# Kernel tuning notes

Hardware: AMD Instinct MI355X
Metric: run time of the kernel (lower is better)

The kernel has to match this reference:

```python
import jax, jax.numpy as jnp
import numpy as np

B, L, DM, H, DH = 2, 2048, 1024, 4, 128
TOT = H * DH  # 512


def _dwconv(x, w, b, L):
    # x: (B,L,C), w: (C,1,4) depthwise, padding=3 then causal trim to L (matches Conv1d(padding=3)[...,:L])
    y = jax.lax.conv_general_dilated(x.transpose(0, 2, 1), w, (1,), [(3, 3)],
                                     dimension_numbers=('NCH', 'OIH', 'NCH'),
                                     feature_group_count=w.shape[0])
    y = y[..., :L] + b[None, :, None]
    return y.transpose(0, 2, 1)


def _l2norm(x):
    return x / jnp.maximum(jnp.linalg.norm(x, axis=-1, keepdims=True), 1e-12)


def setup_inputs() -> dict:
    key = jax.random.key(0)
    ks = jax.random.split(key, 16)
    s = 0.02
    return {
        'x': jax.random.normal(ks[0], (B, L, DM), jnp.float32),
        'state': jnp.zeros((B, H, DH, DH), jnp.float32),
        'Wq': jax.random.normal(ks[1], (TOT, DM), jnp.float32) * s,
        'Wk': jax.random.normal(ks[2], (TOT, DM), jnp.float32) * s,
        'Wv': jax.random.normal(ks[3], (2 * TOT, DM), jnp.float32) * s,
        'Wa': jax.random.normal(ks[4], (H, DM), jnp.float32) * s,
        'Wb': jax.random.normal(ks[5], (H, DM), jnp.float32) * s,
        'Wg': jax.random.normal(ks[6], (TOT, DM), jnp.float32) * s,
        'Wo': jax.random.normal(ks[7], (DM, TOT), jnp.float32) * s,
        'qcw': jax.random.normal(ks[8], (TOT, 1, 4), jnp.float32) * 0.1,
        'qcb': jnp.zeros((TOT,), jnp.float32),
        'kcw': jax.random.normal(ks[9], (TOT, 1, 4), jnp.float32) * 0.1,
        'kcb': jnp.zeros((TOT,), jnp.float32),
        'vcw': jax.random.normal(ks[10], (2 * TOT, 1, 4), jnp.float32) * 0.1,
        'vcb': jnp.zeros((2 * TOT,), jnp.float32),
        'ln_w': jnp.ones((TOT,), jnp.float32),
        'ln_b': jnp.zeros((TOT,), jnp.float32),
    }


def reference(x, state, Wq, Wk, Wv, Wa, Wb, Wg, Wo, qcw, qcb, kcw, kcb, vcw, vcb, ln_w, ln_b):
    Bn, Ln, _ = x.shape
    q = _dwconv(x @ Wq.T, qcw, qcb, Ln)
    k = _dwconv(x @ Wk.T, kcw, kcb, Ln)
    v = _dwconv(x @ Wv.T, vcw, vcb, Ln)
    # silu then L2-normalize over the FULL total_dim (before head split), as in the source
    q = _l2norm(jax.nn.silu(q))
    k = _l2norm(jax.nn.silu(k))
    v = jax.nn.silu(v)
    alpha = jax.nn.sigmoid(x @ Wa.T)  # (B,L,H)
    beta = jax.nn.sigmoid(x @ Wb.T)   # (B,L,H)
    q = q.reshape(Bn, Ln, H, DH)
    k = k.reshape(Bn, Ln, H, DH)
    v_main, v_gate = jnp.split(v, 2, axis=-1)
    v_main = v_main.reshape(Bn, Ln, H, DH)
    v_gate = v_gate.reshape(Bn, Ln, H, DH)

    def step(S, inp):
        q_t, k_t, v_t, a_t, b_t = inp  # (B,H,D),(B,H,D),(B,H,D),(B,H),(B,H)
        a = a_t[..., None, None]
        b = b_t[..., None, None]
        Sk = jnp.einsum('bhij,bhj->bhi', S, k_t)  # S @ k
        # S @ (alpha*(I - beta k k^T)) + beta v k^T, via rank-1 update
        S = a * (S - b * (Sk[..., :, None] * k_t[..., None, :])) \
            + b * (v_t[..., :, None] * k_t[..., None, :])
        o = jnp.einsum('bhij,bhj->bhi', S, q_t)
        return S, o

    xs = (q.transpose(1, 0, 2, 3), k.transpose(1, 0, 2, 3), v_main.transpose(1, 0, 2, 3),
          alpha.transpose(1, 0, 2), beta.transpose(1, 0, 2))
    final_state, outs = jax.lax.scan(step, state, xs)
    out = outs.transpose(1, 0, 2, 3)  # (B,L,H,D)

    out = (out * v_gate).reshape(Bn, Ln, TOT)
    out = out * jax.nn.silu(x @ Wg.T)
    mu = out.mean(-1, keepdims=True)
    var = jnp.mean((out - mu) ** 2, axis=-1, keepdims=True)
    out = (out - mu) * jax.lax.rsqrt(var + 1e-5) * ln_w + ln_b
    out = out @ Wo.T
    return out, final_state
```

## Files before the change

### kernel.cpp

```cpp
#include <hip/hip_runtime.h>
#include <hip/hip_bf16.h>

#define BQ    2
#define LQ    2048
#define DMQ   1024
#define HQ    4
#define DHQ   128
#define TOTQ  512
#define BLQ   4096
#define NPROJ 2688
#define KPROJ 1024
#define CT    64
#define NCH   32

typedef short bf16x8 __attribute__((ext_vector_type(8)));
typedef short s16x4  __attribute__((ext_vector_type(4)));
typedef float f32x4  __attribute__((ext_vector_type(4)));

#define MFMA16(a, b, c) __builtin_amdgcn_mfma_f32_16x16x32_bf16(a, b, c, 0, 0, 0)

__device__ __forceinline__ float siluf(float x) { return x / (1.f + __expf(-x)); }
__device__ __forceinline__ float sigf(float x)  { return 1.f / (1.f + __expf(-x)); }
__device__ __forceinline__ short bf16s(float x) {
  return __builtin_bit_cast(short, __float2bfloat16(x));
}
__device__ __forceinline__ bf16x8 pack8(f32x4 a, f32x4 b) {
  bf16x8 r;
  r[0] = bf16s(a.x); r[1] = bf16s(a.y); r[2] = bf16s(a.z); r[3] = bf16s(a.w);
  r[4] = bf16s(b.x); r[5] = bf16s(b.y); r[6] = bf16s(b.z); r[7] = bf16s(b.w);
  return r;
}

__device__ __forceinline__ void gload_lds16(const void* g, void* l) {
  __builtin_amdgcn_global_load_lds(
      (__attribute__((address_space(1))) void*)(unsigned long long)g,
      (__attribute__((address_space(3))) void*)(unsigned int)(unsigned long long)l,
      16, 0, 0);
}

__global__ __launch_bounds__(256)
void cast_f32_bf16_kernel(const float* __restrict__ src, __hip_bfloat16* __restrict__ dst, int n4)
{
  int i = blockIdx.x * 256 + threadIdx.x;
  if (i < n4) {
    float4 v = ((const float4*)src)[i];
    __hip_bfloat16 o[4] = { __float2bfloat16(v.x), __float2bfloat16(v.y),
                            __float2bfloat16(v.z), __float2bfloat16(v.w) };
    *(ushort4*)((unsigned short*)dst + (size_t)i * 4) = *(ushort4*)o;
  }
}

__global__ __launch_bounds__(256)
void cast_wcat_kernel(const float* __restrict__ Wq, const float* __restrict__ Wk,
                      const float* __restrict__ Wv, const float* __restrict__ Wg,
                      const float* __restrict__ Wa, const float* __restrict__ Wb,
                      __hip_bfloat16* __restrict__ Wcat)
{
  int i4 = blockIdx.x * 256 + threadIdx.x;
  int row = i4 >> 8;
  int col = (i4 & 255) * 4;
  int idx = row * 1024 + col;
  float4 v;
  if      (row < 512)  v = *(const float4*)(Wq + idx);
  else if (row < 1024) v = *(const float4*)(Wk + idx - 512 * 1024);
  else if (row < 2048) v = *(const float4*)(Wv + idx - 1024 * 1024);
  else if (row < 2560) v = *(const float4*)(Wg + idx - 2048 * 1024);
  else if (row < 2564) v = *(const float4*)(Wa + (row - 2560) * 1024 + col);
  else if (row < 2568) v = *(const float4*)(Wb + (row - 2564) * 1024 + col);
  else                 v = make_float4(0.f, 0.f, 0.f, 0.f);
  __hip_bfloat16 o[4] = { __float2bfloat16(v.x), __float2bfloat16(v.y),
                          __float2bfloat16(v.z), __float2bfloat16(v.w) };
  *(ushort4*)((unsigned short*)Wcat + idx) = *(ushort4*)o;
}

__global__ __launch_bounds__(256)
void gemm_bt_kernel(const __hip_bfloat16* __restrict__ A,
                    const __hip_bfloat16* __restrict__ Bw,
                    float* __restrict__ C, int M, int N, int K)
{
  __shared__ __hip_bfloat16 As[2 * 128 * 32];
  __shared__ __hip_bfloat16 Bs[2 * 128 * 32];
  const int tid  = threadIdx.x;
  const int lane = tid & 63;
  const int w    = tid >> 6;
  const int wm   = w >> 1, wn = w & 1;
  const int tm   = blockIdx.x, tn = blockIdx.y;
  const int lr   = lane & 15, lk = lane >> 4;

  f32x4 acc[4][4] = {};

  const int e0   = tid * 8;
  const int srow = e0 >> 5;
  const int scol = e0 & 31;
  const __hip_bfloat16* Ap = A  + (size_t)(tm * 128 + srow) * K + scol;
  const __hip_bfloat16* Bp = Bw + (size_t)(tn * 128 + srow) * K + scol;
  char* AsB  = (char*)As;
  char* BsB  = (char*)Bs;
  const size_t half = (size_t)64 * K;
  const int nk = K >> 5;

  {
    char* AsD = AsB + w * 1024;
    char* BsD = BsB + w * 1024;
    gload_lds16(Ap,        AsD);
    gload_lds16(Ap + half, AsD + 4096);
    gload_lds16(Bp,        BsD);
    gload_lds16(Bp + half, BsD + 4096);
  }
  __syncthreads();

  for (int it = 0; it < nk; ++it) {
    const int sel = it & 1;
    if (it + 1 < nk) {
      const int kk = (it + 1) * 32;
      char* AsD = AsB + ((sel ^ 1) * 8192) + w * 1024;
      char* BsD = BsB + ((sel ^ 1) * 8192) + w * 1024;
      gload_lds16(Ap + kk,        AsD);
      gload_lds16(Ap + half + kk, AsD + 4096);
      gload_lds16(Bp + kk,        BsD);
      gload_lds16(Bp + half + kk, BsD + 4096);
    }
    const char* AsR = AsB + sel * 8192;
    const char* BsR = BsB + sel * 8192;
    bf16x8 af[4], bfv[4];
#pragma unroll
    for (int m = 0; m < 4; ++m)
      af[m]  = *(const bf16x8*)(AsR + ((wm * 64 + m * 16 + lr) * 32 + lk * 8) * 2);
#pragma unroll
    for (int n = 0; n < 4; ++n)
      bfv[n] = *(const bf16x8*)(BsR + ((wn * 64 + n * 16 + lr) * 32 + lk * 8) * 2);
#pragma unroll
    for (int m = 0; m < 4; ++m)
#pragma unroll
      for (int n = 0; n < 4; ++n)
        acc[m][n] = MFMA16(af[m], bfv[n], acc[m][n]);
    __syncthreads();
  }

  const int crow0 = tm * 128 + wm * 64 + (lane >> 4) * 4;
  const int ccol0 = tn * 128 + wn * 64 + lr;
#pragma unroll
  for (int m = 0; m < 4; ++m)
#pragma unroll
    for (int n = 0; n < 4; ++n)
#pragma unroll
      for (int j = 0; j < 4; ++j)
        C[(size_t)(crow0 + m * 16 + j) * N + ccol0 + n * 16] = acc[m][n][j];
}

__global__ __launch_bounds__(256)
void conv_act_kernel(const float* __restrict__ C,
                     const float* __restrict__ qcw, const float* __restrict__ qcb,
                     const float* __restrict__ kcw, const float* __restrict__ kcb,
                     const float* __restrict__ vcw, const float* __restrict__ vcb,
                     float* __restrict__ qh, float* __restrict__ kh,
                     float* __restrict__ vm, float* __restrict__ vg,
                     float* __restrict__ al, float* __restrict__ be)
{
  const int blk = blockIdx.x;
  const int bl0 = blk * 8;
  const int t0  = bl0 & (LQ - 1);
  const int tid = threadIdx.x;
  __shared__ float red[4][16];

  float2 qv[8], kv[8];
  float sq[8], sk[8];
#pragma unroll
  for (int t = 0; t < 8; ++t) { sq[t] = 0.f; sk[t] = 0.f; }

  {
    const int c0 = tid * 2;
    const float4 wqA = *(const float4*)(qcw + 4 * c0);
    const float4 wqB = *(const float4*)(qcw + 4 * c0 + 4);
    const float4 wkA = *(const float4*)(kcw + 4 * c0);
    const float4 wkB = *(const float4*)(kcw + 4 * c0 + 4);
    const float2 bq = *(const float2*)(qcb + c0);
    const float2 bk = *(const float2*)(kcb + c0);
    float2 wrq[11], wrk[11];
#pragma unroll
    for (int r = 0; r < 11; ++r) {
      const int tt = t0 - 3 + r;
      if (tt >= 0) {
        const float* Cr = C + (size_t)(bl0 - 3 + r) * NPROJ;
        wrq[r] = *(const float2*)(Cr + c0);
        wrk[r] = *(const float2*)(Cr + 512 + c0);
      } else {
        wrq[r] = make_float2(0.f, 0.f);
        wrk[r] = make_float2(0.f, 0.f);
      }
    }
#pragma unroll
    for (int t = 0; t < 8; ++t) {
      float aq0 = bq.x, aq1 = bq.y, ak0 = bk.x, ak1 = bk.y;
#pragma unroll
      for (int j = 0; j < 4; ++j) {
        aq0 = fmaf(((const float*)&wqA)[j], wrq[t + j].x, aq0);
        aq1 = fmaf(((const float*)&wqB)[j], wrq[t + j].y, aq1);
        ak0 = fmaf(((const float*)&wkA)[j], wrk[t + j].x, ak0);
        ak1 = fmaf(((const float*)&wkB)[j], wrk[t + j].y, ak1);
      }
      const float q0 = siluf(aq0), q1 = siluf(aq1);
      const float k0 = siluf(ak0), k1 = siluf(ak1);
      qv[t] = make_float2(q0, q1);
      kv[t] = make_float2(k0, k1);
      sq[t] = fmaf(q1, q1, fmaf(q0, q0, sq[t]));
      sk[t] = fmaf(k1, k1, fmaf(k0, k0, sk[t]));
    }
  }
#pragma unroll
  for (int m = 1; m < 64; m <<= 1) {
#pragma unroll
    for (int t = 0; t < 8; ++t) {
      sq[t] += __shfl_xor(sq[t], m);
      sk[t] += __shfl_xor(sk[t], m);
    }
  }
  {
    const int w = tid >> 6, lane = tid & 63;
    if (lane == 0) {
#pragma unroll
      for (int t = 0; t < 8; ++t) { red[w][t] = sq[t]; red[w][8 + t] = sk[t]; }
    }
  }
  __syncthreads();
  float rnq[8], rnk[8];
#pragma unroll
  for (int t = 0; t < 8; ++t) {
    const float SQ = red[0][t] + red[1][t] + red[2][t] + red[3][t];
    const float SK = red[0][8 + t] + red[1][8 + t] + red[2][8 + t] + red[3][8 + t];
    rnq[t] = 1.f / fmaxf(sqrtf(SQ), 1e-12f);
    rnk[t] = 1.f / fmaxf(sqrtf(SK), 1e-12f);
  }
  {
    const int c0 = tid * 2;
#pragma unroll
    for (int t = 0; t < 8; ++t) {
      *(float2*)(qh + (size_t)(bl0 + t) * 512 + c0) =
          make_float2(qv[t].x * rnq[t], qv[t].y * rnq[t]);
      *(float2*)(kh + (size_t)(bl0 + t) * 512 + c0) =
          make_float2(kv[t].x * rnk[t], kv[t].y * rnk[t]);
    }
  }
  {
    const int cv = tid * 4;
    const float4 wv0 = *(const float4*)(vcw + 4 * cv);
    const float4 wv1 = *(const float4*)(vcw + 4 * cv + 4);
    const float4 wv2 = *(const float4*)(vcw + 4 * cv + 8);
    const float4 wv3 = *(const float4*)(vcw + 4 * cv + 12);
    const float4 bv4 = *(const float4*)(vcb + cv);
    float4 wr[11];
#pragma unroll
    for (int r = 0; r < 11; ++r) {
      const int tt = t0 - 3 + r;
      wr[r] = (tt >= 0) ? *(const float4*)(C + (size_t)(bl0 - 3 + r) * NPROJ + 1024 + cv)
                        : make_float4(0.f, 0.f, 0.f, 0.f);
    }
#pragma unroll
    for (int t = 0; t < 8; ++t) {
      float a0 = bv4.x, a1 = bv4.y, a2 = bv4.z, a3 = bv4.w;
#pragma unroll
      for (int j = 0; j < 4; ++j) {
        a0 = fmaf(((const float*)&wv0)[j], ((const float*)&wr[t + j])[0], a0);
        a1 = fmaf(((const float*)&wv1)[j], ((const float*)&wr[t + j])[1], a1);
        a2 = fmaf(((const float*)&wv2)[j], ((const float*)&wr[t + j])[2], a2);
        a3 = fmaf(((const float*)&wv3)[j], ((const float*)&wr[t + j])[3], a3);
      }
      const float4 o = make_float4(siluf(a0), siluf(a1), siluf(a2), siluf(a3));
      if (cv < 512) *(float4*)(vm + (size_t)(bl0 + t) * 512 + cv)         = o;
      else          *(float4*)(vg + (size_t)(bl0 + t) * 512 + (cv - 512)) = o;
    }
  }
  if (tid < 64) {
    const int t = tid >> 3;
    const int k = tid & 7;
    const float* Cr = C + (size_t)(bl0 + t) * NPROJ;
    if (k < 4) al[(size_t)(bl0 + t) * 4 + k]       = sigf(Cr[2560 + k]);
    else       be[(size_t)(bl0 + t) * 4 + (k - 4)] = sigf(Cr[2564 + (k - 4)]);
  }
}

__global__ __launch_bounds__(256)
void scan_phaseA_kernel(const float* __restrict__ qh, const float* __restrict__ kh,
                        const float* __restrict__ vm, const float* __restrict__ al,
                        const float* __restrict__ be,
                        short* __restrict__ WTB, short* __restrict__ ZB,
                        short* __restrict__ PHB, short* __restrict__ KTB,
                        float* __restrict__ GV, float* __restrict__ GC,
                        short* __restrict__ WTFB, short* __restrict__ ZFB)
{
  __shared__ char sm[83968];
  float* Xl = (float*)(sm);
  __hip_bfloat16* KBl = (__hip_bfloat16*)(sm);
  __hip_bfloat16* QBl = (__hip_bfloat16*)(sm + 17408);
  float* Ll  = (float*)(sm + 65536);
  float* dv  = (float*)(sm + 82944);
  float* bv  = (float*)(sm + 83200);
  float* gbv = (float*)(sm + 83456);
  float* fvs = (float*)(sm + 83712);

  const int cb = blockIdx.x;
  const int bh = cb & 7, c = cb >> 3;
  const int b = bh >> 2, h = bh & 3;
  const int tid = threadIdx.x;
  const int lane = tid & 63;
  const int w = tid >> 6;
  const int lr = lane & 15, lk = lane >> 4;
  const size_t rowbase = (size_t)(b * LQ + c * CT) * 512 + h * 128;

#pragma unroll
  for (int rep = 0; rep < 4; ++rep) {
    const int fid = tid + rep * 256;
    const int r = fid >> 4;
    const int cg = (fid & 15) * 8;
    const float* kp = kh + rowbase + (size_t)r * 512 + cg;
    const float* qp = qh + rowbase + (size_t)r * 512 + cg;
    f32x4 k0 = *(const f32x4*)kp, k1 = *(const f32x4*)(kp + 4);
    f32x4 q0 = *(const f32x4*)qp, q1 = *(const f32x4*)(qp + 4);
    *(bf16x8*)(KBl + r * 136 + cg) = pack8(k0, k1);
    *(bf16x8*)(QBl + r * 136 + cg) = pack8(q0, q1);
  }
  if (w == 0) {
    float la = __logf(al[(size_t)(b * LQ + c * CT + lane) * 4 + h]);
    const float bb = be[(size_t)(b * LQ + c * CT + lane) * 4 + h];
#pragma unroll
    for (int off = 1; off < 64; off <<= 1) {
      const float tv = __shfl_up(la, off, 64);
      if (lane >= off) la += tv;
    }
    const float d63 = __shfl(la, 63, 64);
    dv[lane] = la; bv[lane] = bb; gbv[lane] = bb * __expf(la);
    fvs[lane] = __expf(d63 - la);
    GV[cb * 64 + lane] = __expf(la);
    if (lane == 0) GC[cb] = __expf(d63);
  }
  __syncthreads();

  f32x4 aG[4] = {}, aP[4] = {};
#pragma unroll
  for (int ks = 0; ks < 4; ++ks) {
    bf16x8 bk[4];
#pragma unroll
    for (int nt = 0; nt < 4; ++nt)
      bk[nt] = *(const bf16x8*)(KBl + (nt * 16 + lr) * 136 + ks * 32 + lk * 8);
    const bf16x8 ak = *(const bf16x8*)(KBl + (w * 16 + lr) * 136 + ks * 32 + lk * 8);
    const bf16x8 aq = *(const bf16x8*)(QBl + (w * 16 + lr) * 136 + ks * 32 + lk * 8);
#pragma unroll
    for (int nt = 0; nt < 4; ++nt) {
      aG[nt] = MFMA16(ak, bk[nt], aG[nt]);
      aP[nt] = MFMA16(aq, bk[nt], aP[nt]);
    }
  }
#pragma unroll
  for (int nt = 0; nt < 4; ++nt)
#pragma unroll
    for (int jj = 0; jj < 4; ++jj) {
      const int t = w * 16 + lk * 4 + jj;
      const int s = nt * 16 + lr;
      const float eg = __expf(dv[t] - dv[s]);
      Ll[t * 68 + s] = (t > s) ? bv[t] * eg * aG[nt][jj] : 0.f;
      PHB[(size_t)cb * 4096 + t * 64 + s] = (s <= t) ? bf16s(eg * aP[nt][jj]) : (short)0;
    }
  __syncthreads();

  const int j = tid;
  const float* src = (j < 128) ? kh : vm;
  const float* xp = src + rowbase + (j & 127);
  float* XlC = Xl + j;
  short* dstN = (j < 128) ? (WTB + (size_t)cb * 8192 + j)
                          : (ZB  + (size_t)cb * 8192 + (j - 128));
  short* dstT = (j < 128) ? (WTFB + (size_t)cb * 8192 + (size_t)j * 64)
                          : (ZFB  + (size_t)cb * 8192 + (size_t)(j - 128) * 64);

  for (int r = 0; r < 4; ++r) {
    float u[16];
#pragma unroll
    for (int i = 0; i < 16; ++i) {
      const int t = r * 16 + i;
      u[i] = xp[(size_t)t * 512] * ((j < 128) ? gbv[t] : bv[t]);
    }
    for (int sc = 0; sc < r; ++sc) {
      float xs[16];
#pragma unroll
      for (int k = 0; k < 16; ++k) xs[k] = XlC[(sc * 16 + k) * 256];
#pragma unroll
      for (int i = 0; i < 16; ++i) {
        const float* lrow = Ll + (r * 16 + i) * 68 + sc * 16;
        const f32x4 l0 = *(const f32x4*)(lrow);
        const f32x4 l1 = *(const f32x4*)(lrow + 4);
        const f32x4 l2 = *(const f32x4*)(lrow + 8);
        const f32x4 l3 = *(const f32x4*)(lrow + 12);
        f32x4 acc = {};
        acc.x = fmaf(l0.x, xs[0],  acc.x); acc.y = fmaf(l0.y, xs[1],  acc.y);
        acc.z = fmaf(l0.z, xs[2],  acc.z); acc.w = fmaf(l0.w, xs[3],  acc.w);
        acc.x = fmaf(l1.x, xs[4],  acc.x); acc.y = fmaf(l1.y, xs[5],  acc.y);
        acc.z = fmaf(l1.z, xs[6],  acc.z); acc.w = fmaf(l1.w, xs[7],  acc.w);
        acc.x = fmaf(l2.x, xs[8],  acc.x); acc.y = fmaf(l2.y, xs[9],  acc.y);
        acc.z = fmaf(l2.z, xs[10], acc.z); acc.w = fmaf(l2.w, xs[11], acc.w);
        acc.x = fmaf(l3.x, xs[12], acc.x); acc.y = fmaf(l3.y, xs[13], acc.y);
        acc.z = fmaf(l3.z, xs[14], acc.z); acc.w = fmaf(l3.w, xs[15], acc.w);
        u[i] -= (acc.x + acc.y) + (acc.z + acc.w);
      }
    }
#pragma unroll
    for (int i = 1; i < 16; ++i) {
      const float* lrow = Ll + (r * 16 + i) * 68 + r * 16;
      f32x4 acc = {};
#pragma unroll
      for (int k4 = 0; k4 < 4; ++k4) {
        if (k4 * 4 < i) {
          const f32x4 lv = *(const f32x4*)(lrow + k4 * 4);
          acc.x = fmaf(lv.x, u[k4 * 4 + 0], acc.x);
          acc.y = fmaf(lv.y, u[k4 * 4 + 1], acc.y);
          acc.z = fmaf(lv.z, u[k4 * 4 + 2], acc.z);
          acc.w = fmaf(lv.w, u[k4 * 4 + 3], acc.w);
        }
      }
      u[i] -= (acc.x + acc.y) + (acc.z + acc.w);
    }
    if (r < 3) {
#pragma unroll
      for (int i = 0; i < 16; ++i) XlC[(r * 16 + i) * 256] = u[i];
    }
#pragma unroll
    for (int i = 0; i < 16; ++i)
      dstN[(r * 16 + i) * 128] = bf16s(u[i]);
#pragma unroll
    for (int s4 = 0; s4 < 4; ++s4) {
      s16x4 p;
#pragma unroll
      for (int e = 0; e < 4; ++e)
        p[e] = bf16s(fvs[r * 16 + s4 * 4 + e] * u[s4 * 4 + e]);
      *(s16x4*)(dstT + r * 16 + s4 * 4) = p;
    }
  }

  if (tid < 128) {
    const float* kp2 = kh + rowbase + tid;
#pragma unroll
    for (int s4 = 0; s4 < 16; ++s4) {
      s16x4 pk;
#pragma unroll
      for (int e = 0; e < 4; ++e)
        pk[e] = bf16s(kp2[(size_t)(s4 * 4 + e) * 512]);
      *(s16x4*)(KTB + (size_t)cb * 8192 + tid * 64 + s4 * 4) = pk;
    }
  }
}

__global__ __launch_bounds__(256)
void scan_transition_kernel(const short* __restrict__ WTFB, const short* __restrict__ ZFB,
                            const short* __restrict__ KTB, const float* __restrict__ GC,
                            short* __restrict__ TRB, float* __restrict__ BF)
{
  const int cb = blockIdx.x;
  const int tid = threadIdx.x, lane = tid & 63, w = tid >> 6;
  const int lr = lane & 15, lk = lane >> 4;
  const float gc = GC[cb];

  {
    f32x4 acc[2][8] = {};
#pragma unroll
    for (int ks = 0; ks < 2; ++ks) {
      bf16x8 a0 = *(const bf16x8*)(KTB + (size_t)cb * 8192 + (w * 32 + lr) * 64 + ks * 32 + lk * 8);
      bf16x8 a1 = *(const bf16x8*)(KTB + (size_t)cb * 8192 + (w * 32 + 16 + lr) * 64 + ks * 32 + lk * 8);
#pragma unroll
      for (int nt = 0; nt < 8; ++nt) {
        const bf16x8 bm = *(const bf16x8*)(WTFB + (size_t)cb * 8192 + (nt * 16 + lr) * 64 + ks * 32 + lk * 8);
        acc[0][nt] = MFMA16(a0, bm, acc[0][nt]);
        acc[1][nt] = MFMA16(a1, bm, acc[1][nt]);
      }
    }
#pragma unroll
    for (int mt = 0; mt < 2; ++mt)
#pragma unroll
      for (int nt = 0; nt < 8; ++nt)
#pragma unroll
        for (int jj = 0; jj < 4; ++jj) {
          const int jr = w * 32 + mt * 16 + lk * 4 + jj;
          const int m  = nt * 16 + lr;
          const float v = ((jr == m) ? gc : 0.f) - acc[mt][nt][jj];
          TRB[(size_t)cb * 16384 + jr * 128 + m] = bf16s(v);
        }
  }
  {
    f32x4 acc[2][8] = {};
#pragma unroll
    for (int ks = 0; ks < 2; ++ks) {
      bf16x8 a0 = *(const bf16x8*)(ZFB + (size_t)cb * 8192 + (w * 32 + lr) * 64 + ks * 32 + lk * 8);
      bf16x8 a1 = *(const bf16x8*)(ZFB + (size_t)cb * 8192 + (w * 32 + 16 + lr) * 64 + ks * 32 + lk * 8);
#pragma unroll
      for (int nt = 0; nt < 8; ++nt) {
        const bf16x8 bj = *(const bf16x8*)(KTB + (size_t)cb * 8192 + (nt * 16 + lr) * 64 + ks * 32 + lk * 8);
        acc[0][nt] = MFMA16(a0, bj, acc[0][nt]);
        acc[1][nt] = MFMA16(a1, bj, acc[1][nt]);
      }
    }
#pragma unroll
    for (int mt = 0; mt < 2; ++mt)
#pragma unroll
      for (int nt = 0; nt < 8; ++nt)
#pragma unroll
        for (int jj = 0; jj < 4; ++jj) {
          const int ir = w * 32 + mt * 16 + lk * 4 + jj;
          const int jc = nt * 16 + lr;
          BF[(size_t)cb * 16384 + ir * 128 + jc] = acc[mt][nt][jj];
        }
  }
}

#define L2_PREFETCH(BT, BA, CC) do {                                               \
  const int cbn_ = (CC) * 8 + bh;                                                  \
  _Pragma("unroll") for (int nt = 0; nt < 2; ++nt) {                               \
    _Pragma("unroll") for (int ks = 0; ks < 4; ++ks)                               \
      BT[nt][ks] = *(const bf16x8*)(TRB + (size_t)cbn_ * 16384 +                   \
                                    (w * 32 + nt * 16 + lr) * 128 + ks * 32 + lk * 8); \
    _Pragma("unroll") for (int jj = 0; jj < 4; ++jj)                               \
      BA[nt][jj] = BF[(size_t)cbn_ * 16384 + (r0 + lk * 4 + jj) * 128 +            \
                      w * 32 + nt * 16 + lr];                                      \
  }                                                                                \
} while (0)

#define L2_STEP(BT, BA, CC, PBT, PBA) do {                                         \
  const int cb_ = (CC) * 8 + bh;                                                   \
  { const int idx = tid * 8, r = idx >> 7, jc = idx & 127;                         \
    f32x4 s0 = *(const f32x4*)&Scur[r * 132 + jc];                                 \
    f32x4 s1 = *(const f32x4*)&Scur[r * 132 + jc + 4];                             \
    *(bf16x8*)(SALL + (size_t)cb_ * 16384 + (r0 + r) * 128 + jc) = pack8(s0, s1); }\
  bf16x8 af[4];                                                                    \
  _Pragma("unroll") for (int ks = 0; ks < 4; ++ks)                                 \
    af[ks] = pack8(*(const f32x4*)&Scur[lr * 132 + ks * 32 + lk * 8],              \
                   *(const f32x4*)&Scur[lr * 132 + ks * 32 + lk * 8 + 4]);         \
  if ((CC) < 31) L2_PREFETCH(PBT, PBA, (CC) + 1);                                  \
  f32x4 acc0 = {}, acc1 = {};                                                      \
  _Pragma("unroll") for (int ks = 0; ks < 4; ++ks) {                               \
    acc0 = MFMA16(af[ks], BT[0][ks], acc0);                                        \
    acc1 = MFMA16(af[ks], BT[1][ks], acc1);                                        \
  }                                                                                \
  _Pragma("unroll") for (int jj = 0; jj < 4; ++jj) {                               \
    Snxt[(lk * 4 + jj) * 132 + w * 32 + lr]      = acc0[jj] + BA[0][jj];           \
    Snxt[(lk * 4 + jj) * 132 + w * 32 + 16 + lr] = acc1[jj] + BA[1][jj];           \
  }                                                                                \
  __syncthreads();                                                                 \
  { float* t_ = Scur; Scur = Snxt; Snxt = t_; }                                    \
} while (0)

__global__ __launch_bounds__(256)
void scan_state_kernel(const short* __restrict__ TRB, const float* __restrict__ BF,
                       const float* __restrict__ st0, short* __restrict__ SALL,
                       float* __restrict__ stout)
{
  __shared__ float Sl[2 * 16 * 132];
  const int bid = blockIdx.x;
  const int bh = bid & 7, slab = bid >> 3;
  const int r0 = slab * 16;
  const int tid = threadIdx.x, lane = tid & 63, w = tid >> 6;
  const int lr = lane & 15, lk = lane >> 4;

  float* Scur = Sl;
  float* Snxt = Sl + 16 * 132;

  {
    const int idx = tid * 8, r = idx >> 7, jc = idx & 127;
    const float* sp = st0 + ((size_t)bh * 128 + r0 + r) * 128 + jc;
    *(f32x4*)&Scur[r * 132 + jc]     = *(const f32x4*)sp;
    *(f32x4*)&Scur[r * 132 + jc + 4] = *(const f32x4*)(sp + 4);
  }
  bf16x8 btA[2][4], btB[2][4];
  float  baA[2][4], baB[2][4];
  L2_PREFETCH(btA, baA, 0);
  __syncthreads();

  for (int c2 = 0; c2 < 16; ++c2) {
    L2_STEP(btA, baA, 2 * c2,     btB, baB);
    L2_STEP(btB, baB, 2 * c2 + 1, btA, baA);
  }

  {
    const int idx = tid * 8, r = idx >> 7, jc = idx & 127;
    float* sp = stout + ((size_t)bh * 128 + r0 + r) * 128 + jc;
    *(f32x4*)sp       = *(const f32x4*)&Scur[r * 132 + jc];
    *(f32x4*)(sp + 4) = *(const f32x4*)&Scur[r * 132 + jc + 4];
  }
}

__global__ __launch_bounds__(512)
void scan_output_kernel(const float* __restrict__ qh,
                        const short* __restrict__ WTB, const __hip_bfloat16* __restrict__ ZB,
                        const short* __restrict__ PHB, const float* __restrict__ GV,
                        const short* __restrict__ SALL, float* __restrict__ obuf)
{
  __shared__ short Ut[128 * 72];
  const int cb = blockIdx.x;
  const int bh = cb & 7, c = cb >> 3;
  const int b = bh >> 2, h = bh & 3;
  const int tid = threadIdx.x, lane = tid & 63, w = tid >> 6;
  const int lr = lane & 15, lk = lane >> 4;
  const int r0 = (w & 3) * 16;

  f32x4 Y[8] = {};
#pragma unroll
  for (int ks = 0; ks < 4; ++ks) {
    bf16x8 af;
    if (w < 4) {
      const float* qp = qh + ((size_t)(b * LQ + c * CT) + r0 + lr) * 512 + h * 128 + ks * 32 + lk * 8;
      af = pack8(*(const f32x4*)qp, *(const f32x4*)(qp + 4));
    } else {
      af = *(const bf16x8*)(WTB + (size_t)cb * 8192 + (r0 + lr) * 128 + ks * 32 + lk * 8);
    }
#pragma unroll
    for (int nt = 0; nt < 8; ++nt) {
      const bf16x8 bs = *(const bf16x8*)(SALL + (size_t)cb * 16384 + (nt * 16 + lr) * 128 + ks * 32 + lk * 8);
      Y[nt] = MFMA16(af, bs, Y[nt]);
    }
  }
  if (w >= 4) {
#pragma unroll
    for (int nt = 0; nt < 8; ++nt) {
      const int i = nt * 16 + lr;
      s16x4 up;
#pragma unroll
      for (int jj = 0; jj < 4; ++jj) {
        const int s = r0 + lk * 4 + jj;
        const float z = __bfloat162float(ZB[(size_t)cb * 8192 + s * 128 + i]);
        up[jj] = bf16s(z - Y[nt][jj]);
      }
      *(s16x4*)&Ut[i * 72 + r0 + lk * 4] = up;
    }
  }
  __syncthreads();
  if (w < 4) {
    f32x4 P2[8] = {};
#pragma unroll
    for (int ks = 0; ks < 2; ++ks) {
      const bf16x8 ap = *(const bf16x8*)(PHB + (size_t)cb * 4096 + (r0 + lr) * 64 + ks * 32 + lk * 8);
#pragma unroll
      for (int nt = 0; nt < 8; ++nt) {
        const bf16x8 bu = *(const bf16x8*)&Ut[(nt * 16 + lr) * 72 + ks * 32 + lk * 8];
        P2[nt] = MFMA16(ap, bu, P2[nt]);
      }
    }
    float gvv[4];
#pragma unroll
    for (int jj = 0; jj < 4; ++jj) gvv[jj] = GV[cb * 64 + r0 + lk * 4 + jj];
#pragma unroll
    for (int nt = 0; nt < 8; ++nt) {
      const int i = nt * 16 + lr;
#pragma unroll
      for (int jj = 0; jj < 4; ++jj) {
        const int t = r0 + lk * 4 + jj;
        obuf[((size_t)(b * LQ + c * CT) + t) * 512 + h * 128 + i] =
            gvv[jj] * Y[nt][jj] + P2[nt][jj];
      }
    }
  }
}

__global__ __launch_bounds__(256)
void gate_ln_kernel(const float* __restrict__ obuf, const float* __restrict__ vg,
                    const float* __restrict__ C, const float* __restrict__ lnw,
                    const float* __restrict__ lnb, __hip_bfloat16* __restrict__ lno)
{
  const int bl = blockIdx.x, tid = threadIdx.x;
  const int c0 = tid * 2;
  __shared__ float red[8];
  const float2 ov = *(const float2*)(obuf + (size_t)bl * 512 + c0);
  const float2 gv2 = *(const float2*)(vg + (size_t)bl * 512 + c0);
  const float2 gg = *(const float2*)(C + (size_t)bl * NPROJ + 2048 + c0);
  const float v0 = ov.x * gv2.x * siluf(gg.x);
  const float v1 = ov.y * gv2.y * siluf(gg.y);
  float s = v0 + v1;
  float s2 = fmaf(v1, v1, v0 * v0);
  float2 pr = make_float2(s, s2);
#pragma unroll
  for (int m = 1; m < 64; m <<= 1) { pr.x += __shfl_xor(pr.x, m); pr.y += __shfl_xor(pr.y, m); }
  if ((tid & 63) == 0) { red[(tid >> 6) * 2] = pr.x; red[(tid >> 6) * 2 + 1] = pr.y; }
  __syncthreads();
  const float S  = red[0] + red[2] + red[4] + red[6];
  const float S2 = red[1] + red[3] + red[5] + red[7];
  const float mu  = S * (1.f / 512.f);
  const float var = S2 * (1.f / 512.f) - mu * mu;
  const float rs  = rsqrtf(var + 1e-5f);
  const float2 lw = *(const float2*)(lnw + c0);
  const float2 lb = *(const float2*)(lnb + c0);
  __hip_bfloat16 o[2] = {
    __float2bfloat16(fmaf((v0 - mu) * rs, lw.x, lb.x)),
    __float2bfloat16(fmaf((v1 - mu) * rs, lw.y, lb.y)) };
  *(ushort2*)((unsigned short*)lno + (size_t)bl * 512 + c0) = *(ushort2*)o;
}

extern "C" void kernel_launch(void* const* d_in, const int* in_sizes, int n_in,
                              void* d_out, int out_size, void* d_ws, size_t ws_size,
                              hipStream_t stream)
{
  (void)in_sizes; (void)n_in; (void)out_size; (void)ws_size;
  const float* x    = (const float*)d_in[0];
  const float* st0  = (const float*)d_in[1];
  const float* Wq   = (const float*)d_in[2];
  const float* Wk   = (const float*)d_in[3];
  const float* Wv   = (const float*)d_in[4];
  const float* Wa   = (const float*)d_in[5];
  const float* Wb   = (const float*)d_in[6];
  const float* Wg   = (const float*)d_in[7];
  const float* Wo   = (const float*)d_in[8];
  const float* qcw  = (const float*)d_in[9];
  const float* qcb  = (const float*)d_in[10];
  const float* kcw  = (const float*)d_in[11];
  const float* kcb  = (const float*)d_in[12];
  const float* vcw  = (const float*)d_in[13];
  const float* vcb  = (const float*)d_in[14];
  const float* lnw  = (const float*)d_in[15];
  const float* lnb  = (const float*)d_in[16];
  float* out = (float*)d_out;

  char* ws = (char*)d_ws;
  __hip_bfloat16* XB   = (__hip_bfloat16*)(ws + 0);
  __hip_bfloat16* LNO  = (__hip_bfloat16*)(ws + 0);
  short*          WTFB = (short*)(ws + 0);
  short*          WTB  = (short*)(ws + 4194304);
  __hip_bfloat16* WCAT = (__hip_bfloat16*)(ws + 8388608);
  __hip_bfloat16* WOB  = (__hip_bfloat16*)(ws + 13893632);
  float* CBUF = (float*)(ws + 14942208);
  float* QH   = (float*)(ws + 58982400);
  float* KH   = (float*)(ws + 67371008);
  float* BF   = (float*)(ws + 67371008);
  float* VM   = (float*)(ws + 75759616);
  float* VG   = (float*)(ws + 84148224);
  float* AL   = (float*)(ws + 92536832);
  float* BE   = (float*)(ws + 92602368);
  float* OBUF = (float*)(ws + 92667904);
  short* TRB  = (short*)(ws + 92667904);
  short* KTB  = (short*)(ws + 101056512);
  short* PHB  = (short*)(ws + 105250816);
  short* ZB   = (short*)(ws + 107347968);
  float* GV   = (float*)(ws + 111542272);
  float* GC   = (float*)(ws + 111673344);
  short* ZFB  = (short*)(ws + 111674368);
  short* SALL = (short*)(ws + 115868672);

  cast_f32_bf16_kernel<<<4096, 256, 0, stream>>>(x,  XB,  1048576);
  cast_f32_bf16_kernel<<<512,  256, 0, stream>>>(Wo, WOB, 131072);
  cast_wcat_kernel<<<2688, 256, 0, stream>>>(Wq, Wk, Wv, Wg, Wa, Wb, WCAT);

  gemm_bt_kernel<<<dim3(32, 21), 256, 0, stream>>>(XB, WCAT, CBUF, BLQ, NPROJ, KPROJ);

  conv_act_kernel<<<512, 256, 0, stream>>>(CBUF, qcw, qcb, kcw, kcb, vcw, vcb,
                                           QH, KH, VM, VG, AL, BE);

  scan_phaseA_kernel<<<256, 256, 0, stream>>>(QH, KH, VM, AL, BE,
                                              WTB, ZB, PHB, KTB, GV, GC, WTFB, ZFB);

  scan_transition_kernel<<<256, 256, 0, stream>>>(WTFB, ZFB, KTB, GC, TRB, BF);

  scan_state_kernel<<<64, 256, 0, stream>>>(TRB, BF, st0, SALL, out + 4194304);

  scan_output_kernel<<<256, 512, 0, stream>>>(QH, WTB, (const __hip_bfloat16*)ZB,
                                              PHB, GV, SALL, OBUF);

  gate_ln_kernel<<<BLQ, 256, 0, stream>>>(OBUF, VG, CBUF, lnw, lnb, LNO);

  gemm_bt_kernel<<<dim3(32, 8), 256, 0, stream>>>(LNO, WOB, out, BLQ, DMQ, TOTQ);
}
```

Baseline: 166.0 us.

## Store projection and activation intermediates in bf16 to cut memory traffic

The projection GEMM now writes its output in bf16 instead of fp32, with the alpha/beta logit columns also written to a small fp32 side buffer. The conv/activation kernel reads bf16 and writes q, k, v_main and v_gate as bf16. The scan and gate/LN kernels consume bf16 directly, which removes their pack/convert steps. This roughly halves intermediate global-memory traffic, in exchange for extra rounding of pre-conv projections and of the normalized q/k.

```diff
diff --git a/kernel.cpp b/kernel.cpp
--- a/kernel.cpp
+++ b/kernel.cpp
@@ -23,6 +23,9 @@
 __device__ __forceinline__ float sigf(float x)  { return 1.f / (1.f + __expf(-x)); }
 __device__ __forceinline__ short bf16s(float x) {
   return __builtin_bit_cast(short, __float2bfloat16(x));
+}
+__device__ __forceinline__ float bfu2f(unsigned short u) {
+  return __bfloat162float(__builtin_bit_cast(__hip_bfloat16, u));
 }
 __device__ __forceinline__ bf16x8 pack8(f32x4 a, f32x4 b) {
   bf16x8 r;
@@ -73,10 +76,12 @@
   *(ushort4*)((unsigned short*)Wcat + idx) = *(ushort4*)o;
 }
 
+template <typename TOUT>
 __global__ __launch_bounds__(256)
 void gemm_bt_kernel(const __hip_bfloat16* __restrict__ A,
                     const __hip_bfloat16* __restrict__ Bw,
-                    float* __restrict__ C, int M, int N, int K)
+                    TOUT* __restrict__ C, int M, int N, int K,
+                    float* __restrict__ aux, int auxc0)
 {
   __shared__ __hip_bfloat16 As[2 * 128 * 32];
   __shared__ __hip_bfloat16 Bs[2 * 128 * 32];
@@ -142,25 +147,36 @@
 #pragma unroll
   for (int m = 0; m < 4; ++m)
 #pragma unroll
-    for (int n = 0; n < 4; ++n)
-#pragma unroll
-      for (int j = 0; j < 4; ++j)
-        C[(size_t)(crow0 + m * 16 + j) * N + ccol0 + n * 16] = acc[m][n][j];
+    for (int n = 0; n < 4; ++n) {
+      const int cc = ccol0 + n * 16;
+#pragma unroll
+      for (int j = 0; j < 4; ++j) {
+        const float v = acc[m][n][j];
+        const size_t row = (size_t)(crow0 + m * 16 + j);
+        if constexpr (sizeof(TOUT) == 2)
+          ((unsigned short*)C)[row * N + cc] = (unsigned short)bf16s(v);
+        else
+          C[row * N + cc] = v;
+        if (aux && cc >= auxc0 && cc < auxc0 + 8)
+          aux[row * 8 + (cc - auxc0)] = v;
+      }
+    }
 }
 
 __global__ __launch_bounds__(256)
-void conv_act_kernel(const float* __restrict__ C,
+void conv_act_kernel(const __hip_bfloat16* __restrict__ C, const float* __restrict__ abf,
                      const float* __restrict__ qcw, const float* __restrict__ qcb,
                      const float* __restrict__ kcw, const float* __restrict__ kcb,
                      const float* __restrict__ vcw, const float* __restrict__ vcb,
-                     float* __restrict__ qh, float* __restrict__ kh,
-                     float* __restrict__ vm, float* __restrict__ vg,
+                     __hip_bfloat16* __restrict__ qh, __hip_bfloat16* __restrict__ kh,
+                     __hip_bfloat16* __restrict__ vm, __hip_bfloat16* __restrict__ vg,
                      float* __restrict__ al, float* __restrict__ be)
 {
   const int blk = blockIdx.x;
   const int bl0 = blk * 8;
   const int t0  = bl0 & (LQ - 1);
   const int tid = threadIdx.x;
+  const unsigned short* Cu = (const unsigned short*)C;
   __shared__ float red[4][16];
 
   float2 qv[8], kv[8];
@@ -181,9 +197,11 @@
     for (int r = 0; r < 11; ++r) {
       const int tt = t0 - 3 + r;
       if (tt >= 0) {
-        const float* Cr = C + (size_t)(bl0 - 3 + r) * NPROJ;
-        wrq[r] = *(const float2*)(Cr + c0);
-        wrk[r] = *(const float2*)(Cr + 512 + c0);
+        const unsigned short* Cr = Cu + (size_t)(bl0 - 3 + r) * NPROJ;
+        const ushort2 aq = *(const ushort2*)(Cr + c0);
+        const ushort2 ak = *(const ushort2*)(Cr + 512 + c0);
+        wrq[r] = make_float2(bfu2f(aq.x), bfu2f(aq.y));
+        wrk[r] = make_float2(bfu2f(ak.x), bfu2f(ak.y));
       } else {
         wrq[r] = make_float2(0.f, 0.f);
         wrk[r] = make_float2(0.f, 0.f);
@@ -235,10 +253,13 @@
     const int c0 = tid * 2;
 #pragma unroll
     for (int t = 0; t < 8; ++t) {
-      *(float2*)(qh + (size_t)(bl0 + t) * 512 + c0) =
-          make_float2(qv[t].x * rnq[t], qv[t].y * rnq[t]);
-      *(float2*)(kh + (size_t)(bl0 + t) * 512 + c0) =
-          make_float2(kv[t].x * rnk[t], kv[t].y * rnk[t]);
+      ushort2 oq, ok;
+      oq.x = (unsigned short)bf16s(qv[t].x * rnq[t]);
+      oq.y = (unsigned short)bf16s(qv[t].y * rnq[t]);
+      ok.x = (unsigned short)bf16s(kv[t].x * rnk[t]);
+      ok.y = (unsigned short)bf16s(kv[t].y * rnk[t]);
+      *(ushort2*)((unsigned short*)qh + (size_t)(bl0 + t) * 512 + c0) = oq;
+      *(ushort2*)((unsigned short*)kh + (size_t)(bl0 + t) * 512 + c0) = ok;
     }
   }
   {
@@ -252,8 +273,12 @@
 #pragma unroll
     for (int r = 0; r < 11; ++r) {
       const int tt = t0 - 3 + r;
-      wr[r] = (tt >= 0) ? *(const float4*)(C + (size_t)(bl0 - 3 + r) * NPROJ + 1024 + cv)
-                        : make_float4(0.f, 0.f, 0.f, 0.f);
+      if (tt >= 0) {
+        const ushort4 u = *(const ushort4*)(Cu + (size_t)(bl0 - 3 + r) * NPROJ + 1024 + cv);
+        wr[r] = make_float4(bfu2f(u.x), bfu2f(u.y), bfu2f(u.z), bfu2f(u.w));
+      } else {
+        wr[r] = make_float4(0.f, 0.f, 0.f, 0.f);
+      }
     }
 #pragma unroll
     for (int t = 0; t < 8; ++t) {
@@ -265,23 +290,27 @@
         a2 = fmaf(((const float*)&wv2)[j], ((const float*)&wr[t + j])[2], a2);
         a3 = fmaf(((const float*)&wv3)[j], ((const float*)&wr[t + j])[3], a3);
       }
-      const float4 o = make_float4(siluf(a0), siluf(a1), siluf(a2), siluf(a3));
-      if (cv < 512) *(float4*)(vm + (size_t)(bl0 + t) * 512 + cv)         = o;
-      else          *(float4*)(vg + (size_t)(bl0 + t) * 512 + (cv - 512)) = o;
+      ushort4 o;
+      o.x = (unsigned short)bf16s(siluf(a0));
+      o.y = (unsigned short)bf16s(siluf(a1));
+      o.z = (unsigned short)bf16s(siluf(a2));
+      o.w = (unsigned short)bf16s(siluf(a3));
+      if (cv < 512) *(ushort4*)((unsigned short*)vm + (size_t)(bl0 + t) * 512 + cv)         = o;
+      else          *(ushort4*)((unsigned short*)vg + (size_t)(bl0 + t) * 512 + (cv - 512)) = o;
     }
   }
   if (tid < 64) {
     const int t = tid >> 3;
     const int k = tid & 7;
-    const float* Cr = C + (size_t)(bl0 + t) * NPROJ;
-    if (k < 4) al[(size_t)(bl0 + t) * 4 + k]       = sigf(Cr[2560 + k]);
-    else       be[(size_t)(bl0 + t) * 4 + (k - 4)] = sigf(Cr[2564 + (k - 4)]);
+    const float v = abf[(size_t)(bl0 + t) * 8 + k];
+    if (k < 4) al[(size_t)(bl0 + t) * 4 + k]       = sigf(v);
+    else       be[(size_t)(bl0 + t) * 4 + (k - 4)] = sigf(v);
   }
 }
 
 __global__ __launch_bounds__(256)
-void scan_phaseA_kernel(const float* __restrict__ qh, const float* __restrict__ kh,
-                        const float* __restrict__ vm, const float* __restrict__ al,
+void scan_phaseA_kernel(const __hip_bfloat16* __restrict__ qh, const __hip_bfloat16* __restrict__ kh,
+                        const __hip_bfloat16* __restrict__ vm, const float* __restrict__ al,
                         const float* __restrict__ be,
                         short* __restrict__ WTB, short* __restrict__ ZB,
                         short* __restrict__ PHB, short* __restrict__ KTB,
@@ -312,12 +341,8 @@
     const int fid = tid + rep * 256;
     const int r = fid >> 4;
     const int cg = (fid & 15) * 8;
-    const float* kp = kh + rowbase + (size_t)r * 512 + cg;
-    const float* qp = qh + rowbase + (size_t)r * 512 + cg;
-    f32x4 k0 = *(const f32x4*)kp, k1 = *(const f32x4*)(kp + 4);
-    f32x4 q0 = *(const f32x4*)qp, q1 = *(const f32x4*)(qp + 4);
-    *(bf16x8*)(KBl + r * 136 + cg) = pack8(k0, k1);
-    *(bf16x8*)(QBl + r * 136 + cg) = pack8(q0, q1);
+    *(bf16x8*)(KBl + r * 136 + cg) = *(const bf16x8*)(kh + rowbase + (size_t)r * 512 + cg);
+    *(bf16x8*)(QBl + r * 136 + cg) = *(const bf16x8*)(qh + rowbase + (size_t)r * 512 + cg);
   }
   if (w == 0) {
     float la = __logf(al[(size_t)(b * LQ + c * CT + lane) * 4 + h]);
@@ -363,8 +388,8 @@
   __syncthreads();
 
   const int j = tid;
-  const float* src = (j < 128) ? kh : vm;
-  const float* xp = src + rowbase + (j & 127);
+  const __hip_bfloat16* src = (j < 128) ? kh : vm;
+  const __hip_bfloat16* xp = src + rowbase + (j & 127);
   float* XlC = Xl + j;
   short* dstN = (j < 128) ? (WTB + (size_t)cb * 8192 + j)
                           : (ZB  + (size_t)cb * 8192 + (j - 128));
@@ -376,7 +401,7 @@
 #pragma unroll
     for (int i = 0; i < 16; ++i) {
       const int t = r * 16 + i;
-      u[i] = xp[(size_t)t * 512] * ((j < 128) ? gbv[t] : bv[t]);
+      u[i] = __bfloat162float(xp[(size_t)t * 512]) * ((j < 128) ? gbv[t] : bv[t]);
     }
     for (int sc = 0; sc < r; ++sc) {
       float xs[16];
@@ -435,13 +460,13 @@
   }
 
   if (tid < 128) {
-    const float* kp2 = kh + rowbase + tid;
+    const short* kp2 = (const short*)kh + rowbase + tid;
 #pragma unroll
     for (int s4 = 0; s4 < 16; ++s4) {
       s16x4 pk;
 #pragma unroll
       for (int e = 0; e < 4; ++e)
-        pk[e] = bf16s(kp2[(size_t)(s4 * 4 + e) * 512]);
+        pk[e] = kp2[(size_t)(s4 * 4 + e) * 512];
       *(s16x4*)(KTB + (size_t)cb * 8192 + tid * 64 + s4 * 4) = pk;
     }
   }
@@ -584,7 +609,7 @@
 }
 
 __global__ __launch_bounds__(512)
-void scan_output_kernel(const float* __restrict__ qh,
+void scan_output_kernel(const __hip_bfloat16* __restrict__ qh,
                         const short* __restrict__ WTB, const __hip_bfloat16* __restrict__ ZB,
                         const short* __restrict__ PHB, const float* __restrict__ GV,
                         const short* __restrict__ SALL, float* __restrict__ obuf)
@@ -602,8 +627,7 @@
   for (int ks = 0; ks < 4; ++ks) {
     bf16x8 af;
     if (w < 4) {
-      const float* qp = qh + ((size_t)(b * LQ + c * CT) + r0 + lr) * 512 + h * 128 + ks * 32 + lk * 8;
-      af = pack8(*(const f32x4*)qp, *(const f32x4*)(qp + 4));
+      af = *(const bf16x8*)(qh + ((size_t)(b * LQ + c * CT) + r0 + lr) * 512 + h * 128 + ks * 32 + lk * 8);
     } else {
       af = *(const bf16x8*)(WTB + (size_t)cb * 8192 + (r0 + lr) * 128 + ks * 32 + lk * 8);
     }
@@ -656,18 +680,18 @@
 }
 
 __global__ __launch_bounds__(256)
-void gate_ln_kernel(const float* __restrict__ obuf, const float* __restrict__ vg,
-                    const float* __restrict__ C, const float* __restrict__ lnw,
+void gate_ln_kernel(const float* __restrict__ obuf, const __hip_bfloat16* __restrict__ vg,
+                    const __hip_bfloat16* __restrict__ C, const float* __restrict__ lnw,
                     const float* __restrict__ lnb, __hip_bfloat16* __restrict__ lno)
 {
   const int bl = blockIdx.x, tid = threadIdx.x;
   const int c0 = tid * 2;
   __shared__ float red[8];
   const float2 ov = *(const float2*)(obuf + (size_t)bl * 512 + c0);
-  const float2 gv2 = *(const float2*)(vg + (size_t)bl * 512 + c0);
-  const float2 gg = *(const float2*)(C + (size_t)bl * NPROJ + 2048 + c0);
-  const float v0 = ov.x * gv2.x * siluf(gg.x);
-  const float v1 = ov.y * gv2.y * siluf(gg.y);
+  const ushort2 gvu = *(const ushort2*)((const unsigned short*)vg + (size_t)bl * 512 + c0);
+  const ushort2 ggu = *(const ushort2*)((const unsigned short*)C + (size_t)bl * NPROJ + 2048 + c0);
+  const float v0 = ov.x * bfu2f(gvu.x) * siluf(bfu2f(ggu.x));
+  const float v1 = ov.y * bfu2f(gvu.y) * siluf(bfu2f(ggu.y));
   float s = v0 + v1;
   float s2 = fmaf(v1, v1, v0 * v0);
   float2 pr = make_float2(s, s2);
@@ -719,12 +743,12 @@
   short*          WTB  = (short*)(ws + 4194304);
   __hip_bfloat16* WCAT = (__hip_bfloat16*)(ws + 8388608);
   __hip_bfloat16* WOB  = (__hip_bfloat16*)(ws + 13893632);
-  float* CBUF = (float*)(ws + 14942208);
-  float* QH   = (float*)(ws + 58982400);
-  float* KH   = (float*)(ws + 67371008);
+  __hip_bfloat16* CBUFH = (__hip_bfloat16*)(ws + 14942208);
+  __hip_bfloat16* QH   = (__hip_bfloat16*)(ws + 58982400);
+  __hip_bfloat16* KH   = (__hip_bfloat16*)(ws + 67371008);
   float* BF   = (float*)(ws + 67371008);
-  float* VM   = (float*)(ws + 75759616);
-  float* VG   = (float*)(ws + 84148224);
+  __hip_bfloat16* VM   = (__hip_bfloat16*)(ws + 75759616);
+  __hip_bfloat16* VG   = (__hip_bfloat16*)(ws + 84148224);
   float* AL   = (float*)(ws + 92536832);
   float* BE   = (float*)(ws + 92602368);
   float* OBUF = (float*)(ws + 92667904);
@@ -736,14 +760,16 @@
   float* GC   = (float*)(ws + 111673344);
   short* ZFB  = (short*)(ws + 111674368);
   short* SALL = (short*)(ws + 115868672);
+  float* ABF  = (float*)(ws + 124257280);
 
   cast_f32_bf16_kernel<<<4096, 256, 0, stream>>>(x,  XB,  1048576);
   cast_f32_bf16_kernel<<<512,  256, 0, stream>>>(Wo, WOB, 131072);
   cast_wcat_kernel<<<2688, 256, 0, stream>>>(Wq, Wk, Wv, Wg, Wa, Wb, WCAT);
 
-  gemm_bt_kernel<<<dim3(32, 21), 256, 0, stream>>>(XB, WCAT, CBUF, BLQ, NPROJ, KPROJ);
-
-  conv_act_kernel<<<512, 256, 0, stream>>>(CBUF, qcw, qcb, kcw, kcb, vcw, vcb,
+  gemm_bt_kernel<__hip_bfloat16><<<dim3(32, 21), 256, 0, stream>>>(
+      XB, WCAT, CBUFH, BLQ, NPROJ, KPROJ, ABF, 2560);
+
+  conv_act_kernel<<<512, 256, 0, stream>>>(CBUFH, ABF, qcw, qcb, kcw, kcb, vcw, vcb,
                                            QH, KH, VM, VG, AL, BE);
 
   scan_phaseA_kernel<<<256, 256, 0, stream>>>(QH, KH, VM, AL, BE,
@@ -756,7 +782,8 @@
   scan_output_kernel<<<256, 512, 0, stream>>>(QH, WTB, (const __hip_bfloat16*)ZB,
                                               PHB, GV, SALL, OBUF);
 
-  gate_ln_kernel<<<BLQ, 256, 0, stream>>>(OBUF, VG, CBUF, lnw, lnb, LNO);
-
-  gemm_bt_kernel<<<dim3(32, 8), 256, 0, stream>>>(LNO, WOB, out, BLQ, DMQ, TOTQ);
-}
+  gate_ln_kernel<<<BLQ, 256, 0, stream>>>(OBUF, VG, CBUFH, lnw, lnb, LNO);
+
+  gemm_bt_kernel<float><<<dim3(32, 8), 256, 0, stream>>>(
+      LNO, WOB, out, BLQ, DMQ, TOTQ, nullptr, 0);
+}
```

New measurement: 159.3 us. 1.04x faster.
